# Optimization experiments

Measured on AMD Instinct MI355X. Metric: run time of the kernel, lower is better.

Reference implementation:

```python
import jax, jax.numpy as jnp
import numpy as np


def setup_inputs() -> dict:
    key = jax.random.key(0)
    kx, kd = jax.random.split(key)
    B, T, C = 32, 512, 512
    x = jax.random.normal(kx, (B, T, C), dtype=jnp.float32)
    dur = jax.random.randint(kd, (B, T), 0, 12, dtype=jnp.int32)
    return {"x": x, "dur": dur}


def reference(x, dur):
    # x: [B, T, C]; dur: [B, T] integer per-token durations.
    # Equivalent of the torch CPU double-loop: output frame t of row b
    # takes source index j where cumsum(dur)[b, j-1] <= t < cumsum(dur)[b, j];
    # frames past the total duration repeat the last source index (T-1).
    dur = jnp.maximum(dur, 0)
    cum = jnp.cumsum(dur, axis=1)                       # [B, T], nondecreasing
    T_out = int(jnp.max(cum))                            # data-dependent output length (eager)
    frames = jnp.arange(T_out, dtype=cum.dtype)          # [T_out]
    # searchsorted(cum[b], t, 'right') == first j with cum[b, j] > t
    idx = jax.vmap(lambda c: jnp.searchsorted(c, frames, side="right"))(cum)  # [B, T_out]
    idx = jnp.minimum(idx, x.shape[1] - 1)               # overflow -> last token, matches torch loop
    return jnp.take_along_axis(x, idx[:, :, None], axis=1)  # [B, T_out, C]
```

## Files before the change

kernel.cpp:

```cpp
#include <hip/hip_runtime.h>
#include <hip/hip_bf16.h>


#define LR_T 512

__global__ void lr_cumsum_kernel(const int* __restrict__ dur,
                                 int* __restrict__ cum, int T) {
    __shared__ int s[LR_T];
    const int b = blockIdx.x;
    const int t = threadIdx.x;
    int v = dur[(size_t)b * T + t];
    v = v > 0 ? v : 0;
    s[t] = v;
    __syncthreads();
    for (int off = 1; off < LR_T; off <<= 1) {
        int add = (t >= off) ? s[t - off] : 0;
        __syncthreads();
        s[t] += add;
        __syncthreads();
    }
    cum[(size_t)b * T + t] = s[t];
}

__global__ void lr_gather_kernel(const float* __restrict__ x,
                                 const int* __restrict__ cum,
                                 float* __restrict__ out,
                                 int T, int T_out, int C) {
    const int t = blockIdx.x;
    const int b = blockIdx.y;

    const int* crow = cum + (size_t)b * T;
    int lo = 0, hi = T;
    while (lo < hi) {
        int mid = (lo + hi) >> 1;
        if (crow[mid] > t) hi = mid; else lo = mid + 1;
    }
    int idx = lo < (T - 1) ? lo : (T - 1);

    const float4* __restrict__ src =
        (const float4*)(x + ((size_t)b * T + idx) * C);
    float4* __restrict__ dst =
        (float4*)(out + ((size_t)b * T_out + t) * C);
    dst[threadIdx.x] = src[threadIdx.x];
}

extern "C" void kernel_launch(void* const* d_in, const int* in_sizes, int n_in,
                              void* d_out, int out_size, void* d_ws, size_t ws_size,
                              hipStream_t stream) {
    const float* x   = (const float*)d_in[0];
    const int*   dur = (const int*)d_in[1];
    float*       out = (float*)d_out;

    const int B  = 32;
    const int BT = in_sizes[1];
    const int T  = BT / B;
    const int C  = in_sizes[0] / BT;
    const int T_out = out_size / (B * C);

    int* cum = (int*)d_ws;

    lr_cumsum_kernel<<<B, T, 0, stream>>>(dur, cum, T);

    dim3 grid(T_out, B);
    lr_gather_kernel<<<grid, C / 4, 0, stream>>>(x, cum, out, T, T_out, C);
}
```

Measured before the change: 255.0 us.

## Precompute per-frame source offsets in scan kernel and use flat grid-stride copy

The binary search moves out of the gather into the cumsum kernel, which searches shared memory and writes a per-frame source row offset table. The gather becomes a flat grid-stride float4 copy capped at 8192 blocks of 256 threads. This removes the redundant global-memory binary search done by every 128-thread block and the large number of small blocks. In exchange, the index kernel runs on only 32 blocks doing serial searches, the copy needs an extra table lookup per element, and the shift/mask indexing assumes C/4 is a power of two.

```diff
diff --git a/kernel.cpp b/kernel.cpp
--- a/kernel.cpp
+++ b/kernel.cpp
@@ -4,44 +4,49 @@
 
 #define LR_T 512
 
-__global__ void lr_cumsum_kernel(const int* __restrict__ dur,
-                                 int* __restrict__ cum, int T) {
+__global__ void lr_index_kernel(const int* __restrict__ dur,
+                                int* __restrict__ srcoff,
+                                int T, int T_out) {
     __shared__ int s[LR_T];
     const int b = blockIdx.x;
-    const int t = threadIdx.x;
-    int v = dur[(size_t)b * T + t];
+    const int tid = threadIdx.x;
+
+    int v = dur[(size_t)b * T + tid];
     v = v > 0 ? v : 0;
-    s[t] = v;
+    s[tid] = v;
     __syncthreads();
     for (int off = 1; off < LR_T; off <<= 1) {
-        int add = (t >= off) ? s[t - off] : 0;
+        int add = (tid >= off) ? s[tid - off] : 0;
         __syncthreads();
-        s[t] += add;
+        s[tid] += add;
         __syncthreads();
     }
-    cum[(size_t)b * T + t] = s[t];
+
+    int* rowmap = srcoff + (size_t)b * T_out;
+    const int base = b * T;
+    for (int t = tid; t < T_out; t += LR_T) {
+        int lo = 0, hi = T;
+        while (lo < hi) {
+            int mid = (lo + hi) >> 1;
+            if (s[mid] > t) hi = mid; else lo = mid + 1;
+        }
+        int idx = lo < (T - 1) ? lo : (T - 1);
+        rowmap[t] = base + idx;
+    }
 }
 
-__global__ void lr_gather_kernel(const float* __restrict__ x,
-                                 const int* __restrict__ cum,
-                                 float* __restrict__ out,
-                                 int T, int T_out, int C) {
-    const int t = blockIdx.x;
-    const int b = blockIdx.y;
-
-    const int* crow = cum + (size_t)b * T;
-    int lo = 0, hi = T;
-    while (lo < hi) {
-        int mid = (lo + hi) >> 1;
-        if (crow[mid] > t) hi = mid; else lo = mid + 1;
+__global__ void lr_copy_kernel(const float4* __restrict__ x4,
+                               const int* __restrict__ srcoff,
+                               float4* __restrict__ out4,
+                               long n4, int c4, int c4shift) {
+    long i = (long)blockIdx.x * blockDim.x + threadIdx.x;
+    const long stride = (long)gridDim.x * blockDim.x;
+    const long mask = c4 - 1;
+    for (; i < n4; i += stride) {
+        const int row = (int)(i >> c4shift);
+        const long lane = i & mask;
+        out4[i] = x4[(size_t)srcoff[row] * c4 + lane];
     }
-    int idx = lo < (T - 1) ? lo : (T - 1);
-
-    const float4* __restrict__ src =
-        (const float4*)(x + ((size_t)b * T + idx) * C);
-    float4* __restrict__ dst =
-        (float4*)(out + ((size_t)b * T_out + t) * C);
-    dst[threadIdx.x] = src[threadIdx.x];
 }
 
 extern "C" void kernel_launch(void* const* d_in, const int* in_sizes, int n_in,
@@ -57,10 +62,18 @@
     const int C  = in_sizes[0] / BT;
     const int T_out = out_size / (B * C);
 
-    int* cum = (int*)d_ws;
+    int* srcoff = (int*)d_ws;
 
-    lr_cumsum_kernel<<<B, T, 0, stream>>>(dur, cum, T);
+    lr_index_kernel<<<B, LR_T, 0, stream>>>(dur, srcoff, T, T_out);
 
-    dim3 grid(T_out, B);
-    lr_gather_kernel<<<grid, C / 4, 0, stream>>>(x, cum, out, T, T_out, C);
+    const long n4 = (long)out_size / 4;
+    const int c4 = C / 4;
+    int c4shift = 0;
+    while ((1 << c4shift) < c4) ++c4shift;
+
+    int threads = 256;
+    long want = (n4 + threads - 1) / threads;
+    int blocks = (int)(want < 8192 ? want : 8192);
+    lr_copy_kernel<<<blocks, threads, 0, stream>>>(
+        (const float4*)x, srcoff, (float4*)out, n4, c4, c4shift);
 }
```

Measured after the change: 239.2 us. 1.07x faster.

## Replace per-frame binary-search gather with per-token scatter of repeated rows

Applied to the files above, without the earlier changes.

The gather kernel, which ran one block per output frame and binary-searched the cumsum row, is replaced by a scatter kernel with one block per source token. Each block loads its row once and writes it to every output frame in its duration range. The last token also fills the tail frames past its cumsum. This removes the per-frame binary search and repeated source reads, but per-block work becomes uneven and zero-duration tokens launch blocks that exit at once. C is hardcoded to 512 (128 float4 lanes).

```diff
diff --git a/kernel.cpp b/kernel.cpp
--- a/kernel.cpp
+++ b/kernel.cpp
@@ -8,40 +8,41 @@
                                  int* __restrict__ cum, int T) {
     __shared__ int s[LR_T];
     const int b = blockIdx.x;
-    const int t = threadIdx.x;
-    int v = dur[(size_t)b * T + t];
+    const int tid = threadIdx.x;
+    int v = dur[(size_t)b * T + tid];
     v = v > 0 ? v : 0;
-    s[t] = v;
+    s[tid] = v;
     __syncthreads();
     for (int off = 1; off < LR_T; off <<= 1) {
-        int add = (t >= off) ? s[t - off] : 0;
+        int add = (tid >= off) ? s[tid - off] : 0;
         __syncthreads();
-        s[t] += add;
+        s[tid] += add;
         __syncthreads();
     }
-    cum[(size_t)b * T + t] = s[t];
+    cum[(size_t)b * T + tid] = s[tid];
 }
 
-__global__ void lr_gather_kernel(const float* __restrict__ x,
-                                 const int* __restrict__ cum,
-                                 float* __restrict__ out,
-                                 int T, int T_out, int C) {
-    const int t = blockIdx.x;
+__global__ void __launch_bounds__(128)
+lr_scatter_kernel(const float4* __restrict__ x4,
+                  const int* __restrict__ cum,
+                  float4* __restrict__ out4,
+                  int T, int T_out) {
+    const int j = blockIdx.x;
     const int b = blockIdx.y;
+    const int tid = threadIdx.x;
 
     const int* crow = cum + (size_t)b * T;
-    int lo = 0, hi = T;
-    while (lo < hi) {
-        int mid = (lo + hi) >> 1;
-        if (crow[mid] > t) hi = mid; else lo = mid + 1;
+    int start = (j > 0) ? crow[j - 1] : 0;
+    int end   = (j == T - 1) ? T_out : crow[j];
+    if (start >= end) return;
+
+    const float4 val = x4[((size_t)b * T + j) * 128 + tid];
+
+    float4* dst = out4 + ((size_t)b * T_out + start) * 128 + tid;
+    for (int t = start; t < end; ++t) {
+        *dst = val;
+        dst += 128;
     }
-    int idx = lo < (T - 1) ? lo : (T - 1);
-
-    const float4* __restrict__ src =
-        (const float4*)(x + ((size_t)b * T + idx) * C);
-    float4* __restrict__ dst =
-        (float4*)(out + ((size_t)b * T_out + t) * C);
-    dst[threadIdx.x] = src[threadIdx.x];
 }
 
 extern "C" void kernel_launch(void* const* d_in, const int* in_sizes, int n_in,
@@ -61,6 +62,7 @@
 
     lr_cumsum_kernel<<<B, T, 0, stream>>>(dur, cum, T);
 
-    dim3 grid(T_out, B);
-    lr_gather_kernel<<<grid, C / 4, 0, stream>>>(x, cum, out, T, T_out, C);
+    dim3 grid(T, B);
+    lr_scatter_kernel<<<grid, 128, 0, stream>>>(
+        (const float4*)x, cum, (float4*)out, T, T_out);
 }
```

After: 246.1 us. 1.04x faster.
